# Kernel optimization log

Measured on AMD Instinct MI355X. Metric: run time of the kernel, lower is better.

Reference implementation:

```python
import jax, jax.numpy as jnp
import numpy as np

BLOCK = 128   # selection_block_size
TOP_K = 16    # top_k per block


def setup_inputs() -> dict:
    key = jax.random.key(0)
    k1, k2 = jax.random.split(key)
    B, S, D = 8, 16384, 512
    x = jax.random.normal(k1, (B, S, D), dtype=jnp.float32)
    W = jax.random.normal(k2, (1, D), dtype=jnp.float32) * (1.0 / np.sqrt(D))
    b = jnp.zeros((1,), dtype=jnp.float32)
    return {"x": x, "W": W, "b": b}


def reference(x, W, b):
    B, S, D = x.shape
    n_blocks = S // BLOCK
    # Linear scoring: [B, S]
    scores = jnp.einsum("bsd,d->bs", x, W[0]) + b[0]
    # Block-wise top-k: reshape to [B, n_blocks, BLOCK]
    block_scores = scores.reshape(B, n_blocks, BLOCK)
    _, top_idx = jax.lax.top_k(block_scores, TOP_K)          # [B, n_blocks, TOP_K]
    # Offset indices back to global sequence positions
    offsets = (jnp.arange(n_blocks, dtype=top_idx.dtype) * BLOCK)[None, :, None]
    sel_idx = (top_idx + offsets).reshape(B, n_blocks * TOP_K)  # [B, n_sel]
    # Gather selected tokens: [B, n_sel, D]
    selected_tokens = jnp.take_along_axis(x, sel_idx[:, :, None], axis=1)
    return selected_tokens
```

## Files before the change

kernel.cpp:

```cpp
#include <hip/hip_runtime.h>

#define B_SZ     8
#define S_SZ     16384
#define D_SZ     512
#define BLK_TOK  128
#define TOPK     16
#define NBLK     (S_SZ / BLK_TOK)

__global__ __launch_bounds__(256, 4) void token_select_kernel(
    const float* __restrict__ x,
    const float* __restrict__ W,
    float* __restrict__ out)
{
    const int blk  = blockIdx.x;
    const int b    = blockIdx.y;
    const int tid  = threadIdx.x;
    const int wave = tid >> 6;
    const int lane = tid & 63;

    __shared__ double s_score[BLK_TOK];
    __shared__ int    s_sel[TOPK];

    const float4* W4 = reinterpret_cast<const float4*>(W);
    const float4 w0 = W4[lane];
    const float4 w1 = W4[64 + lane];

    const float* xbase = x + ((size_t)b * S_SZ + (size_t)blk * BLK_TOK) * D_SZ;

    const int t0 = wave * 32;
    #pragma unroll 4
    for (int t = t0; t < t0 + 32; ++t) {
        const float4* row = reinterpret_cast<const float4*>(xbase + (size_t)t * D_SZ);
        const float4 a0 = row[lane];
        const float4 a1 = row[64 + lane];
        double acc = (double)a0.x * (double)w0.x + (double)a0.y * (double)w0.y
                   + (double)a0.z * (double)w0.z + (double)a0.w * (double)w0.w
                   + (double)a1.x * (double)w1.x + (double)a1.y * (double)w1.y
                   + (double)a1.z * (double)w1.z + (double)a1.w * (double)w1.w;
        #pragma unroll
        for (int m = 32; m >= 1; m >>= 1)
            acc += __shfl_xor(acc, m, 64);
        if (lane == 0) s_score[t] = acc;
    }
    __syncthreads();

    if (wave == 0) {
        double sc0 = s_score[lane];
        double sc1 = s_score[lane + 64];
        #pragma unroll
        for (int k = 0; k < TOPK; ++k) {
            double bs; int bi;
            if (sc0 >= sc1) { bs = sc0; bi = lane; }
            else            { bs = sc1; bi = lane + 64; }
            #pragma unroll
            for (int m = 32; m >= 1; m >>= 1) {
                const double os = __shfl_xor(bs, m, 64);
                const int    oi = __shfl_xor(bi, m, 64);
                if (os > bs || (os == bs && oi < bi)) { bs = os; bi = oi; }
            }
            if (lane == 0) s_sel[k] = bi;
            if (bi == lane)      sc0 = -INFINITY;
            if (bi == lane + 64) sc1 = -INFINITY;
        }
    }
    __syncthreads();

    float* outbase = out + (((size_t)b * NBLK + blk) * TOPK) * D_SZ;
    #pragma unroll
    for (int r = wave; r < TOPK; r += 4) {
        const int idx = s_sel[r];
        const float4* src = reinterpret_cast<const float4*>(xbase + (size_t)idx * D_SZ);
        float4*       dst = reinterpret_cast<float4*>(outbase + (size_t)r * D_SZ);
        dst[lane]      = src[lane];
        dst[64 + lane] = src[64 + lane];
    }
}

extern "C" void kernel_launch(void* const* d_in, const int* in_sizes, int n_in,
                              void* d_out, int out_size, void* d_ws, size_t ws_size,
                              hipStream_t stream) {
    const float* x = (const float*)d_in[0];
    const float* W = (const float*)d_in[1];
    float* out = (float*)d_out;

    dim3 grid(NBLK, B_SZ);
    dim3 block(256);
    token_select_kernel<<<grid, block, 0, stream>>>(x, W, out);
}
```

Measured before the change: 65.43 us.

## Split scoring and top-k gather into separate kernels via workspace scores

```diff
diff --git a/kernel.cpp b/kernel.cpp
--- a/kernel.cpp
+++ b/kernel.cpp
@@ -6,31 +6,29 @@
 #define BLK_TOK  128
 #define TOPK     16
 #define NBLK     (S_SZ / BLK_TOK)
+#define NTOK     (B_SZ * S_SZ)
 
-__global__ __launch_bounds__(256, 4) void token_select_kernel(
+#define TOK_PER_WG   32
+#define TOK_PER_WAVE 8
+
+__global__ __launch_bounds__(256, 8) void score_kernel(
     const float* __restrict__ x,
     const float* __restrict__ W,
-    float* __restrict__ out)
+    double* __restrict__ scores)
 {
-    const int blk  = blockIdx.x;
-    const int b    = blockIdx.y;
     const int tid  = threadIdx.x;
     const int wave = tid >> 6;
     const int lane = tid & 63;
-
-    __shared__ double s_score[BLK_TOK];
-    __shared__ int    s_sel[TOPK];
 
     const float4* W4 = reinterpret_cast<const float4*>(W);
     const float4 w0 = W4[lane];
     const float4 w1 = W4[64 + lane];
 
-    const float* xbase = x + ((size_t)b * S_SZ + (size_t)blk * BLK_TOK) * D_SZ;
+    const int t0 = blockIdx.x * TOK_PER_WG + wave * TOK_PER_WAVE;
 
-    const int t0 = wave * 32;
-    #pragma unroll 4
-    for (int t = t0; t < t0 + 32; ++t) {
-        const float4* row = reinterpret_cast<const float4*>(xbase + (size_t)t * D_SZ);
+    #pragma unroll 2
+    for (int t = t0; t < t0 + TOK_PER_WAVE; ++t) {
+        const float4* row = reinterpret_cast<const float4*>(x + (size_t)t * D_SZ);
         const float4 a0 = row[lane];
         const float4 a1 = row[64 + lane];
         double acc = (double)a0.x * (double)w0.x + (double)a0.y * (double)w0.y
@@ -40,13 +38,28 @@
         #pragma unroll
         for (int m = 32; m >= 1; m >>= 1)
             acc += __shfl_xor(acc, m, 64);
-        if (lane == 0) s_score[t] = acc;
+        if (lane == 0) scores[t] = acc;
     }
-    __syncthreads();
+}
+
+__global__ __launch_bounds__(256, 4) void topk_gather_kernel(
+    const float* __restrict__ x,
+    const double* __restrict__ scores,
+    float* __restrict__ out)
+{
+    const int blk  = blockIdx.x;
+    const int b    = blockIdx.y;
+    const int tid  = threadIdx.x;
+    const int wave = tid >> 6;
+    const int lane = tid & 63;
+
+    __shared__ int s_sel[TOPK];
+
+    const size_t tok0 = (size_t)b * S_SZ + (size_t)blk * BLK_TOK;
 
     if (wave == 0) {
-        double sc0 = s_score[lane];
-        double sc1 = s_score[lane + 64];
+        double sc0 = scores[tok0 + lane];
+        double sc1 = scores[tok0 + 64 + lane];
         #pragma unroll
         for (int k = 0; k < TOPK; ++k) {
             double bs; int bi;
@@ -65,7 +78,8 @@
     }
     __syncthreads();
 
-    float* outbase = out + (((size_t)b * NBLK + blk) * TOPK) * D_SZ;
+    const float* xbase   = x + tok0 * D_SZ;
+    float*       outbase = out + (((size_t)b * NBLK + blk) * TOPK) * D_SZ;
     #pragma unroll
     for (int r = wave; r < TOPK; r += 4) {
         const int idx = s_sel[r];
@@ -81,9 +95,9 @@
                               hipStream_t stream) {
     const float* x = (const float*)d_in[0];
     const float* W = (const float*)d_in[1];
-    float* out = (float*)d_out;
+    float*  out    = (float*)d_out;
+    double* scores = (double*)d_ws;
 
-    dim3 grid(NBLK, B_SZ);
-    dim3 block(256);
-    token_select_kernel<<<grid, block, 0, stream>>>(x, W, out);
+    score_kernel<<<dim3(NTOK / TOK_PER_WG), dim3(256), 0, stream>>>(x, W, scores);
+    topk_gather_kernel<<<dim3(NBLK, B_SZ), dim3(256), 0, stream>>>(x, scores, out);
 }
```

Measured after the change: 68.16 us. +4.2%, slower.

## Use 512-thread blocks, rank-based top-k selection, and two-row scoring per iteration

Applied to the files above, without the earlier changes.

```diff
diff --git a/kernel.cpp b/kernel.cpp
--- a/kernel.cpp
+++ b/kernel.cpp
@@ -7,7 +7,7 @@
 #define TOPK     16
 #define NBLK     (S_SZ / BLK_TOK)
 
-__global__ __launch_bounds__(256, 4) void token_select_kernel(
+__global__ __launch_bounds__(512, 8) void token_select_kernel(
     const float* __restrict__ x,
     const float* __restrict__ W,
     float* __restrict__ out)
@@ -27,47 +27,50 @@
 
     const float* xbase = x + ((size_t)b * S_SZ + (size_t)blk * BLK_TOK) * D_SZ;
 
-    const int t0 = wave * 32;
-    #pragma unroll 4
-    for (int t = t0; t < t0 + 32; ++t) {
-        const float4* row = reinterpret_cast<const float4*>(xbase + (size_t)t * D_SZ);
-        const float4 a0 = row[lane];
-        const float4 a1 = row[64 + lane];
-        double acc = (double)a0.x * (double)w0.x + (double)a0.y * (double)w0.y
-                   + (double)a0.z * (double)w0.z + (double)a0.w * (double)w0.w
-                   + (double)a1.x * (double)w1.x + (double)a1.y * (double)w1.y
-                   + (double)a1.z * (double)w1.z + (double)a1.w * (double)w1.w;
+    const int t0 = wave * 16;
+    for (int t = t0; t < t0 + 16; t += 2) {
+        const float4* r0 = reinterpret_cast<const float4*>(xbase + (size_t)t * D_SZ);
+        const float4* r1 = reinterpret_cast<const float4*>(xbase + (size_t)(t + 1) * D_SZ);
+        const float4 a0 = r0[lane];
+        const float4 a1 = r0[64 + lane];
+        const float4 c0 = r1[lane];
+        const float4 c1 = r1[64 + lane];
+
+        double accA = (double)a0.x * (double)w0.x + (double)a0.y * (double)w0.y
+                    + (double)a0.z * (double)w0.z + (double)a0.w * (double)w0.w
+                    + (double)a1.x * (double)w1.x + (double)a1.y * (double)w1.y
+                    + (double)a1.z * (double)w1.z + (double)a1.w * (double)w1.w;
+        double accB = (double)c0.x * (double)w0.x + (double)c0.y * (double)w0.y
+                    + (double)c0.z * (double)w0.z + (double)c0.w * (double)w0.w
+                    + (double)c1.x * (double)w1.x + (double)c1.y * (double)w1.y
+                    + (double)c1.z * (double)w1.z + (double)c1.w * (double)w1.w;
         #pragma unroll
-        for (int m = 32; m >= 1; m >>= 1)
-            acc += __shfl_xor(acc, m, 64);
-        if (lane == 0) s_score[t] = acc;
+        for (int m = 32; m >= 1; m >>= 1) {
+            accA += __shfl_xor(accA, m, 64);
+            accB += __shfl_xor(accB, m, 64);
+        }
+        if (lane == 0) {
+            s_score[t]     = accA;
+            s_score[t + 1] = accB;
+        }
     }
     __syncthreads();
 
-    if (wave == 0) {
-        double sc0 = s_score[lane];
-        double sc1 = s_score[lane + 64];
-        #pragma unroll
-        for (int k = 0; k < TOPK; ++k) {
-            double bs; int bi;
-            if (sc0 >= sc1) { bs = sc0; bi = lane; }
-            else            { bs = sc1; bi = lane + 64; }
-            #pragma unroll
-            for (int m = 32; m >= 1; m >>= 1) {
-                const double os = __shfl_xor(bs, m, 64);
-                const int    oi = __shfl_xor(bi, m, 64);
-                if (os > bs || (os == bs && oi < bi)) { bs = os; bi = oi; }
-            }
-            if (lane == 0) s_sel[k] = bi;
-            if (bi == lane)      sc0 = -INFINITY;
-            if (bi == lane + 64) sc1 = -INFINITY;
+    if (tid < BLK_TOK) {
+        const double mine = s_score[tid];
+        int rank = 0;
+        #pragma unroll 8
+        for (int j = 0; j < BLK_TOK; ++j) {
+            const double sj = s_score[j];
+            rank += (sj > mine) || (sj == mine && j < tid);
         }
+        if (rank < TOPK) s_sel[rank] = tid;
     }
     __syncthreads();
 
     float* outbase = out + (((size_t)b * NBLK + blk) * TOPK) * D_SZ;
     #pragma unroll
-    for (int r = wave; r < TOPK; r += 4) {
+    for (int r = wave * 2; r < wave * 2 + 2; ++r) {
         const int idx = s_sel[r];
         const float4* src = reinterpret_cast<const float4*>(xbase + (size_t)idx * D_SZ);
         float4*       dst = reinterpret_cast<float4*>(outbase + (size_t)r * D_SZ);
@@ -83,7 +86,5 @@
     const float* W = (const float*)d_in[1];
     float* out = (float*)d_out;
 
-    dim3 grid(NBLK, B_SZ);
-    dim3 block(256);
-    token_select_kernel<<<grid, block, 0, stream>>>(x, W, out);
+    token_select_kernel<<<dim3(NBLK, B_SZ), dim3(512), 0, stream>>>(x, W, out);
 }
```

Result: no change. 64.62 us (-1.2%).
